# Kernel optimization log

Hardware: AMD Instinct MI355X
Metric: run time of the kernel (lower is better)

Reference implementation:

```python
import jax, jax.numpy as jnp
import numpy as np

B, S, D, H, F = 4, 2048, 1024, 16, 4096
DH = D // H
EPS = 1e-6


def setup_inputs() -> dict:
    key = jax.random.key(0)
    ks = jax.random.split(key, 8)
    sc = 1.0 / np.sqrt(D)
    return {
        "x": jax.random.normal(ks[0], (B, S, D), jnp.float32),
        "wq": jax.random.normal(ks[1], (D, D), jnp.float32) * sc,
        "bq": jnp.zeros((D,), jnp.float32),
        "wk": jax.random.normal(ks[2], (D, D), jnp.float32) * sc,
        "bk": jnp.zeros((D,), jnp.float32),
        "wv": jax.random.normal(ks[3], (D, D), jnp.float32) * sc,
        "bv": jnp.zeros((D,), jnp.float32),
        "wo": jax.random.normal(ks[4], (D, D), jnp.float32) * sc,
        "bo": jnp.zeros((D,), jnp.float32),
        "w1": jax.random.normal(ks[5], (D, F), jnp.float32) * sc,
        "b1": jnp.zeros((F,), jnp.float32),
        "w2": jax.random.normal(ks[6], (F, D), jnp.float32) * (1.0 / np.sqrt(F)),
        "b2": jnp.zeros((D,), jnp.float32),
        "g1": jnp.ones((D,), jnp.float32),
        "be1": jnp.zeros((D,), jnp.float32),
        "g2": jnp.ones((D,), jnp.float32),
        "be2": jnp.zeros((D,), jnp.float32),
    }


def _layernorm(x, g, b):
    mu = jnp.mean(x, axis=-1, keepdims=True)
    var = jnp.mean(jnp.square(x - mu), axis=-1, keepdims=True)
    return (x - mu) * jax.lax.rsqrt(var + EPS) * g + b


def reference(x, wq, bq, wk, bk, wv, bv, wo, bo, w1, b1, w2, b2, g1, be1, g2, be2):
    # self-attention: q=k=v=x
    q = (x @ wq + bq).reshape(B, S, H, DH).transpose(0, 2, 1, 3)  # [B,H,S,DH]
    k = (x @ wk + bk).reshape(B, S, H, DH).transpose(0, 2, 1, 3)
    v = (x @ wv + bv).reshape(B, S, H, DH).transpose(0, 2, 1, 3)
    logits = jnp.einsum("bhqd,bhkd->bhqk", q, k) / jnp.sqrt(jnp.float32(DH))
    attn = jax.nn.softmax(logits, axis=-1)
    ctx = jnp.einsum("bhqk,bhkd->bhqd", attn, v)  # [B,H,S,DH]
    ctx = ctx.transpose(0, 2, 1, 3).reshape(B, S, D)
    attn_out = ctx @ wo + bo
    out1 = _layernorm(x + attn_out, g1, be1)
    ffn = jax.nn.relu(out1 @ w1 + b1) @ w2 + b2
    out2 = _layernorm(out1 + ffn, g2, be2)
    return out2
```

## Files before the change

kernel.cpp:

```cpp
#include <hip/hip_runtime.h>

typedef unsigned short u16;
typedef unsigned int u32;

typedef __attribute__((ext_vector_type(8))) short short8;
typedef __attribute__((ext_vector_type(4))) float floatx4;
typedef __attribute__((ext_vector_type(16))) float floatx16;
typedef __attribute__((ext_vector_type(2))) unsigned int uint2v;
typedef __attribute__((ext_vector_type(4))) unsigned int uint4v;

static __device__ __forceinline__ u16 f2b(float f) {
    union { float f; u32 i; } v; v.f = f;
    u32 r = v.i + 0x7fffu + ((v.i >> 16) & 1u);
    return (u16)(r >> 16);
}
static __device__ __forceinline__ float exp2f_hw(float x) {
    return __builtin_amdgcn_exp2f(x);
}
static __device__ __forceinline__ u32 cvtpk(float lo, float hi) {
    u32 r;
    asm("v_cvt_pk_bf16_f32 %0, %1, %2" : "=v"(r) : "v"(lo), "v"(hi));
    return r;
}

static __device__ __forceinline__ floatx4 mfma16(short8 a, short8 b, floatx4 c) {
    return __builtin_amdgcn_mfma_f32_16x16x32_bf16(a, b, c, 0, 0, 0);
}
static __device__ __forceinline__ floatx16 mfma32(short8 a, short8 b, floatx16 c) {
    return __builtin_amdgcn_mfma_f32_32x32x16_bf16(a, b, c, 0, 0, 0);
}

typedef __attribute__((address_space(1))) const void gas_void;
typedef __attribute__((address_space(3))) void las_void;
static __device__ __forceinline__ void gl_lds16(const void* g, void* l) {
    __builtin_amdgcn_global_load_lds((gas_void*)g, (las_void*)l, 16, 0, 0);
}

template<int N> static __device__ __forceinline__ void vmw() {
    if constexpr (N == 0)      asm volatile("s_waitcnt vmcnt(0)" ::: "memory");
    else if constexpr (N == 2) asm volatile("s_waitcnt vmcnt(2)" ::: "memory");
    else if constexpr (N == 4) asm volatile("s_waitcnt vmcnt(4)" ::: "memory");
}
#define SBAR() asm volatile("s_barrier" ::: "memory")

#define B_ 4
#define S_ 2048
#define D_ 1024
#define H_ 16
#define DH_ 64
#define F_ 4096
#define QKVS 3072

#define QSCALE 0.18033688011112042f

__global__ __launch_bounds__(256) void cast_b(const float* __restrict__ in,
                                              u16* __restrict__ out, int n4) {
    int id = blockIdx.x * 256 + threadIdx.x;
    if (id < n4) {
        float4 v = ((const float4*)in)[id];
        ushort4 u;
        u.x = f2b(v.x); u.y = f2b(v.y); u.z = f2b(v.z); u.w = f2b(v.w);
        ((ushort4*)out)[id] = u;
    }
}

__global__ __launch_bounds__(256) void concat_bias(const float* __restrict__ bq,
                                                   const float* __restrict__ bk,
                                                   const float* __restrict__ bv,
                                                   float* __restrict__ o) {
    int i = blockIdx.x * 256 + threadIdx.x;
    float v;
    if (i < 1024) v = bq[i] * QSCALE;
    else if (i < 2048) v = bk[i - 1024];
    else v = bv[i - 2048];
    o[i] = v;
}

__global__ void transpose_cast(const float* __restrict__ in, u16* __restrict__ out,
                               int R, int C, float scale) {
    __shared__ float t[32][33];
    int bx = blockIdx.x;
    int by = blockIdx.y;
    int x = threadIdx.x, y = threadIdx.y;
#pragma unroll
    for (int i = 0; i < 4; ++i) {
        int r = by * 32 + y + i * 8;
        t[y + i * 8][x] = in[(size_t)r * C + bx * 32 + x];
    }
    __syncthreads();
#pragma unroll
    for (int i = 0; i < 4; ++i) {
        int c = bx * 32 + y + i * 8;
        out[(size_t)c * R + by * 32 + x] = f2b(t[x][y + i * 8] * scale);
    }
}

__global__ void transpose_v(const u16* __restrict__ qkv, u16* __restrict__ vt) {
    __shared__ u16 t[32][33];
    int bh = blockIdx.z; int b = bh >> 4, h = bh & 15;
    int s0 = blockIdx.x * 32, d0 = blockIdx.y * 32;
    int x = threadIdx.x, y = threadIdx.y;
#pragma unroll
    for (int i = 0; i < 4; ++i)
        t[y + i * 8][x] =
            qkv[(size_t)(b * S_ + s0 + y + i * 8) * QKVS + 2048 + h * DH_ + d0 + x];
    __syncthreads();
#pragma unroll
    for (int i = 0; i < 4; ++i)
        vt[((size_t)bh * DH_ + d0 + y + i * 8) * S_ + s0 + x] = t[x][y + i * 8];
}

#define MFMA16X(MH)                                                        \
    __builtin_amdgcn_s_setprio(1);                                         \
    acc[(MH)*4+0][0] = mfma16(af0, bf0, acc[(MH)*4+0][0]);                 \
    acc[(MH)*4+0][1] = mfma16(af0, bf1, acc[(MH)*4+0][1]);                 \
    acc[(MH)*4+0][2] = mfma16(af0, bf2, acc[(MH)*4+0][2]);                 \
    acc[(MH)*4+0][3] = mfma16(af0, bf3, acc[(MH)*4+0][3]);                 \
    acc[(MH)*4+1][0] = mfma16(af1, bf0, acc[(MH)*4+1][0]);                 \
    acc[(MH)*4+1][1] = mfma16(af1, bf1, acc[(MH)*4+1][1]);                 \
    acc[(MH)*4+1][2] = mfma16(af1, bf2, acc[(MH)*4+1][2]);                 \
    acc[(MH)*4+1][3] = mfma16(af1, bf3, acc[(MH)*4+1][3]);                 \
    acc[(MH)*4+2][0] = mfma16(af2, bf0, acc[(MH)*4+2][0]);                 \
    acc[(MH)*4+2][1] = mfma16(af2, bf1, acc[(MH)*4+2][1]);                 \
    acc[(MH)*4+2][2] = mfma16(af2, bf2, acc[(MH)*4+2][2]);                 \
    acc[(MH)*4+2][3] = mfma16(af2, bf3, acc[(MH)*4+2][3]);                 \
    acc[(MH)*4+3][0] = mfma16(af3, bf0, acc[(MH)*4+3][0]);                 \
    acc[(MH)*4+3][1] = mfma16(af3, bf1, acc[(MH)*4+3][1]);                 \
    acc[(MH)*4+3][2] = mfma16(af3, bf2, acc[(MH)*4+3][2]);                 \
    acc[(MH)*4+3][3] = mfma16(af3, bf3, acc[(MH)*4+3][3]);                 \
    __builtin_amdgcn_s_setprio(0);

#define PPAIR(P, KH, STa, Wa, STb, Wb) {                                   \
    int ro = l * 64 + ((((KH) * 4 + quad) ^ l7) << 3);                     \
    const u16* bBp = &smem[32768 + (P) * 16384 + wc * 4096];               \
    short8 bf0 = *(const short8*)&bBp[ro];                                 \
    short8 bf1 = *(const short8*)&bBp[ro + 1024];                          \
    short8 bf2 = *(const short8*)&bBp[ro + 2048];                          \
    short8 bf3 = *(const short8*)&bBp[ro + 3072];                          \
    {   const u16* bAp = &smem[(P) * 16384 + (wr * 2 + 0) * 4096];         \
        short8 af0 = *(const short8*)&bAp[ro];                             \
        short8 af1 = *(const short8*)&bAp[ro + 1024];                      \
        short8 af2 = *(const short8*)&bAp[ro + 2048];                      \
        short8 af3 = *(const short8*)&bAp[ro + 3072];                      \
        STa; Wa;                                                           \
        MFMA16X(0)                                                         \
        SBAR();                                                            \
    }                                                                      \
    {   const u16* bAp = &smem[(P) * 16384 + (wr * 2 + 1) * 4096];         \
        short8 af0 = *(const short8*)&bAp[ro];                             \
        short8 af1 = *(const short8*)&bAp[ro + 1024];                      \
        short8 af2 = *(const short8*)&bAp[ro + 2048];                      \
        short8 af3 = *(const short8*)&bAp[ro + 3072];                      \
        STb; Wb;                                                           \
        MFMA16X(1)                                                         \
        SBAR();                                                            \
    } }

__global__ __launch_bounds__(512) void gemm256(const u16* __restrict__ A,
                                               const u16* __restrict__ Bt,
                                               const float* __restrict__ bias,
                                               float* __restrict__ outF,
                                               float* __restrict__ outF2,
                                               u16* __restrict__ outB,
                                               int M, int N, int K, int klen,
                                               int relu) {
    __shared__ __align__(16) u16 smem[65536];

    int tid = threadIdx.x;
    int w = tid >> 6, lane = tid & 63, quad = lane >> 4, l = lane & 15;
    int wr = w >> 2, wc = w & 3;
    int l7 = l & 7;

    int nbN = gridDim.x, nwg = gridDim.x * gridDim.y;
    int flat = blockIdx.y * gridDim.x + blockIdx.x;
    int swz = (flat & 7) * (nwg >> 3) + (flat >> 3);
    int bM = swz / nbN, bN = swz % nbN;
    int koff = blockIdx.z * klen;

    floatx4 acc[8][4];
#pragma unroll
    for (int i = 0; i < 8; ++i)
#pragma unroll
        for (int j = 0; j < 4; ++j) acc[i][j] = (floatx4){0.f, 0.f, 0.f, 0.f};

    int rT = tid >> 3, cT = tid & 7;
    int cg8 = ((cT ^ (rT & 7)) << 3);
    const u16* gA0 = A + (size_t)(bM * 256 + rT) * K + koff + cg8;
    const u16* gB0 = Bt + (size_t)(bN * 256 + rT) * K + koff + cg8;

    auto stA = [&](int p, int ch, int t) {
        gl_lds16(gA0 + (size_t)(ch * 64) * K + t * 64,
                 (void*)&smem[p * 16384 + ch * 4096 + (w << 9)]);
    };
    auto stB = [&](int p, int hb, int t) {
        gl_lds16(gB0 + (size_t)(hb * 64) * K + t * 64,
                 (void*)&smem[32768 + p * 16384 + hb * 4096 + (w << 9)]);
    };

    stA(0, 0, 0); stA(0, 1, 0); stA(0, 2, 0); stA(0, 3, 0);
    stB(0, 0, 0); stB(0, 1, 0); stB(0, 2, 0); stB(0, 3, 0);
    stA(1, 0, 1); stA(1, 2, 1);
    vmw<2>(); SBAR();

    const int NI = klen >> 7;
    for (int j = 0; j < NI - 1; ++j) {
        int to = 2 * j + 1, te = 2 * j + 2, tn = 2 * j + 3;
        PPAIR(0, 0, (stA(1,1,to), stA(1,3,to), stB(1,0,to), stB(1,1,to)), ((void)0),
                    (stB(1,2,to), stB(1,3,to)), ((void)0))
        PPAIR(0, 1, ((void)0), ((void)0),
                    (stA(0,0,te), stA(0,2,te)), vmw<2>())
        PPAIR(1, 0, (stA(0,1,te), stA(0,3,te), stB(0,0,te), stB(0,1,te)), ((void)0),
                    (stB(0,2,te), stB(0,3,te)), ((void)0))
        PPAIR(1, 1, ((void)0), ((void)0),
                    (stA(1,0,tn), stA(1,2,tn)), vmw<2>())
    }
    {
        int to = 2 * (NI - 1) + 1;
        PPAIR(0, 0, (stA(1,1,to), stA(1,3,to), stB(1,0,to), stB(1,1,to)), ((void)0),
                    (stB(1,2,to), stB(1,3,to)), ((void)0))
        PPAIR(0, 1, ((void)0), ((void)0), ((void)0), vmw<0>())
        PPAIR(1, 0, ((void)0), ((void)0), ((void)0), ((void)0))
        PPAIR(1, 1, ((void)0), ((void)0), ((void)0), ((void)0))
    }

    float* of = (blockIdx.z == 0) ? outF : outF2;
    const float* bp = (blockIdx.z == 0) ? bias : nullptr;
    float bv4[4];
#pragma unroll
    for (int nt = 0; nt < 4; ++nt) {
        int colg = bN * 256 + wc * 64 + nt * 16 + l;
        bv4[nt] = bp ? bp[colg] : 0.f;
    }
#pragma unroll
    for (int mt = 0; mt < 8; ++mt) {
#pragma unroll
        for (int rr = 0; rr < 4; ++rr) {
            int rowg = bM * 256 + wr * 128 + mt * 16 + quad * 4 + rr;
            size_t rb = (size_t)rowg * N + bN * 256 + wc * 64 + l;
#pragma unroll
            for (int nt = 0; nt < 4; ++nt) {
                float v = acc[mt][nt][rr] + bv4[nt];
                if (relu) v = fmaxf(v, 0.f);
                if (of) of[rb + nt * 16] = v;
                if (outB) outB[rb + nt * 16] = f2b(v);
            }
        }
    }
}

#define PACK8(sv, rb, dst) {                                                   \
    u32 pa_ = cvtpk(sv[rb + 0], sv[rb + 1]), pb_ = cvtpk(sv[rb + 4], sv[rb + 5]); \
    u32 pc_ = cvtpk(sv[rb + 2], sv[rb + 3]), pd_ = cvtpk(sv[rb + 6], sv[rb + 7]); \
    uint2v t0_ = __builtin_amdgcn_permlane32_swap(pa_, pb_, 0, 0);             \
    uint2v t1_ = __builtin_amdgcn_permlane32_swap(pc_, pd_, 0, 0);             \
    union { uint4v u; short8 s8; } cv_;                                        \
    cv_.u = (uint4v){t0_[0], t1_[0], t0_[1], t1_[1]};                          \
    dst = cv_.s8; }

__global__ __launch_bounds__(256, 2) void attn_kernel(const u16* __restrict__ qkv,
                                                      const u16* __restrict__ vt,
                                                      u16* __restrict__ ctx) {
    __shared__ __align__(16) u16 Kb[2][64 * 64];
    __shared__ __align__(16) u16 Vb[2][64 * 64];

    int bh = blockIdx.x; int b = bh >> 4, h = bh & 15;
    int tid = threadIdx.x;
    int w = tid >> 6, lane = tid & 63;
    int l32 = lane & 31, hi = lane >> 5, row7 = lane & 7;
    int qw = blockIdx.y * 256 + w * 64;

    int r = lane >> 3, c = lane & 7;
    int cs = ((c ^ r) << 3);
    const u16* gK0 = qkv + (size_t)(b * S_ + w * 16 + r) * QKVS + 1024 + h * DH_ + cs;
    const u16* gK1 = gK0 + (size_t)8 * QKVS;
    const u16* gV0 = vt + (size_t)(bh * DH_ + w * 16 + r) * S_ + cs;
    const u16* gV1 = gV0 + (size_t)8 * S_;

    auto stage = [&](int bb) {
        u16* lk = &Kb[bb][w * 16 * 64];
        u16* lv = &Vb[bb][w * 16 * 64];
        gl_lds16(gK0, lk);
        gl_lds16(gK1, lk + 8 * 64);
        gl_lds16(gV0, lv);
        gl_lds16(gV1, lv + 8 * 64);
        gK0 += (size_t)64 * QKVS; gK1 += (size_t)64 * QKVS;
        gV0 += 64; gV1 += 64;
    };

    short8 qa0, qa1, qa2, qa3, qb0, qb1, qb2, qb3;
    {
        const u16* qpA = qkv + (size_t)(b * S_ + qw + l32) * QKVS + h * DH_ + hi * 8;
        qa0 = *(const short8*)(qpA);
        qa1 = *(const short8*)(qpA + 16);
        qa2 = *(const short8*)(qpA + 32);
        qa3 = *(const short8*)(qpA + 48);
        const u16* qpB = qpA + (size_t)32 * QKVS;
        qb0 = *(const short8*)(qpB);
        qb1 = *(const short8*)(qpB + 16);
        qb2 = *(const short8*)(qpB + 32);
        qb3 = *(const short8*)(qpB + 48);
    }

    floatx16 OA0, OA1, OB0, OB1;
#pragma unroll
    for (int i = 0; i < 16; ++i) { OA0[i] = 0.f; OA1[i] = 0.f; OB0[i] = 0.f; OB1[i] = 0.f; }
    float lra0 = 0.f, lra1 = 0.f, lrb0 = 0.f, lrb1 = 0.f;

    int roff0 = l32 * 64;
    int roff1 = (32 + l32) * 64;

    stage(0);
    __syncthreads();

    const int NT = S_ / 64;
    for (int kt = 0; kt < NT; ++kt) {
        int cur = kt & 1;
        if (kt + 1 < NT) stage(cur ^ 1);

        const u16* Kc = Kb[cur];
        const u16* Vc = Vb[cur];

        short8 paA0, paA1, paA2, paA3, paB0, paB1, paB2, paB3;

        {
            floatx16 sA, sB;
#pragma unroll
            for (int i = 0; i < 16; ++i) { sA[i] = 0.f; sB[i] = 0.f; }
#pragma unroll
            for (int kc = 0; kc < 4; ++kc) {
                int ch = (((kc * 2 + hi) ^ row7) << 3);
                short8 ka = *(const short8*)&Kc[roff0 + ch];
                short8 qkA = (kc == 0) ? qa0 : (kc == 1) ? qa1 : (kc == 2) ? qa2 : qa3;
                short8 qkB = (kc == 0) ? qb0 : (kc == 1) ? qb1 : (kc == 2) ? qb2 : qb3;
                sA = mfma32(ka, qkA, sA);
                sB = mfma32(ka, qkB, sB);
            }
#pragma unroll
            for (int i = 0; i < 16; ++i) { sA[i] = exp2f_hw(sA[i]); sB[i] = exp2f_hw(sB[i]); }
#pragma unroll
            for (int i = 0; i < 16; i += 4) {
                lra0 += sA[i + 0] + sA[i + 1];
                lra1 += sA[i + 2] + sA[i + 3];
                lrb0 += sB[i + 0] + sB[i + 1];
                lrb1 += sB[i + 2] + sB[i + 3];
            }
            PACK8(sA, 0, paA0); PACK8(sA, 8, paA1);
            PACK8(sB, 0, paB0); PACK8(sB, 8, paB1);
        }

        {
            floatx16 sA, sB;
#pragma unroll
            for (int i = 0; i < 16; ++i) { sA[i] = 0.f; sB[i] = 0.f; }
#pragma unroll
            for (int kc = 0; kc < 4; ++kc) {
                int ch = (((kc * 2 + hi) ^ row7) << 3);
                short8 ka = *(const short8*)&Kc[roff1 + ch];
                short8 qkA = (kc == 0) ? qa0 : (kc == 1) ? qa1 : (kc == 2) ? qa2 : qa3;
                short8 qkB = (kc == 0) ? qb0 : (kc == 1) ? qb1 : (kc == 2) ? qb2 : qb3;
                sA = mfma32(ka, qkA, sA);
                sB = mfma32(ka, qkB, sB);
            }
#pragma unroll
            for (int i = 0; i < 16; ++i) { sA[i] = exp2f_hw(sA[i]); sB[i] = exp2f_hw(sB[i]); }
#pragma unroll
            for (int i = 0; i < 16; i += 4) {
                lra0 += sA[i + 0] + sA[i + 1];
                lra1 += sA[i + 2] + sA[i + 3];
                lrb0 += sB[i + 0] + sB[i + 1];
                lrb1 += sB[i + 2] + sB[i + 3];
            }
            PACK8(sA, 0, paA2); PACK8(sA, 8, paA3);
            PACK8(sB, 0, paB2); PACK8(sB, 8, paB3);
        }

        {
            short8 vb0 = *(const short8*)&Vc[roff0 + (((0 + hi) ^ row7) << 3)];
            OA0 = mfma32(paA0, vb0, OA0);
            OB0 = mfma32(paB0, vb0, OB0);
            short8 vb1 = *(const short8*)&Vc[roff0 + (((2 + hi) ^ row7) << 3)];
            OA0 = mfma32(paA1, vb1, OA0);
            OB0 = mfma32(paB1, vb1, OB0);
            short8 vb2 = *(const short8*)&Vc[roff0 + (((4 + hi) ^ row7) << 3)];
            OA0 = mfma32(paA2, vb2, OA0);
            OB0 = mfma32(paB2, vb2, OB0);
            short8 vb3 = *(const short8*)&Vc[roff0 + (((6 + hi) ^ row7) << 3)];
            OA0 = mfma32(paA3, vb3, OA0);
            OB0 = mfma32(paB3, vb3, OB0);
        }
        {
            short8 vb0 = *(const short8*)&Vc[roff1 + (((0 + hi) ^ row7) << 3)];
            OA1 = mfma32(paA0, vb0, OA1);
            OB1 = mfma32(paB0, vb0, OB1);
            short8 vb1 = *(const short8*)&Vc[roff1 + (((2 + hi) ^ row7) << 3)];
            OA1 = mfma32(paA1, vb1, OA1);
            OB1 = mfma32(paB1, vb1, OB1);
            short8 vb2 = *(const short8*)&Vc[roff1 + (((4 + hi) ^ row7) << 3)];
            OA1 = mfma32(paA2, vb2, OA1);
            OB1 = mfma32(paB2, vb2, OB1);
            short8 vb3 = *(const short8*)&Vc[roff1 + (((6 + hi) ^ row7) << 3)];
            OA1 = mfma32(paA3, vb3, OA1);
            OB1 = mfma32(paB3, vb3, OB1);
        }

        __syncthreads();
    }

    float lrA = lra0 + lra1;
    float lrB = lrb0 + lrb1;
    lrA += __shfl_xor(lrA, 32);
    lrB += __shfl_xor(lrB, 32);
    float invA = 1.0f / lrA;
    float invB = 1.0f / lrB;
#pragma unroll
    for (int rr = 0; rr < 16; ++rr) {
        int rowq = (rr & 3) + 8 * (rr >> 2) + 4 * hi;
        float ivA = __shfl(invA, rowq);
        float ivB = __shfl(invB, rowq);
        size_t baseA = (size_t)(b * S_ + qw + rowq) * D_ + h * DH_ + l32;
        ctx[baseA]      = f2b(OA0[rr] * ivA);
        ctx[baseA + 32] = f2b(OA1[rr] * ivA);
        size_t baseB = baseA + (size_t)32 * D_;
        ctx[baseB]      = f2b(OB0[rr] * ivB);
        ctx[baseB + 32] = f2b(OB1[rr] * ivB);
    }
}

__global__ __launch_bounds__(256) void add_ln(const float* __restrict__ a,
                                              const float* __restrict__ b,
                                              const float* __restrict__ g,
                                              const float* __restrict__ be,
                                              float* __restrict__ outF,
                                              u16* __restrict__ outB) {
    int row = blockIdx.x, tid = threadIdx.x;
    size_t base = (size_t)row * D_;
    float4 va = ((const float4*)(a + base))[tid];
    float4 vb = ((const float4*)(b + base))[tid];
    float x0 = va.x + vb.x, x1 = va.y + vb.y, x2 = va.z + vb.z, x3 = va.w + vb.w;
    float s1 = x0 + x1 + x2 + x3;
    float s2 = x0 * x0 + x1 * x1 + x2 * x2 + x3 * x3;
#pragma unroll
    for (int off = 32; off; off >>= 1) {
        s1 += __shfl_xor(s1, off);
        s2 += __shfl_xor(s2, off);
    }
    __shared__ float r1[4], r2[4];
    int w = tid >> 6, lane = tid & 63;
    if (lane == 0) { r1[w] = s1; r2[w] = s2; }
    __syncthreads();
    s1 = r1[0] + r1[1] + r1[2] + r1[3];
    s2 = r2[0] + r2[1] + r2[2] + r2[3];
    float mean = s1 * (1.0f / D_);
    float var = s2 * (1.0f / D_) - mean * mean;
    float inv = rsqrtf(var + 1e-6f);
    float4 vg = ((const float4*)g)[tid];
    float4 vbe = ((const float4*)be)[tid];
    float o0 = (x0 - mean) * inv * vg.x + vbe.x;
    float o1 = (x1 - mean) * inv * vg.y + vbe.y;
    float o2 = (x2 - mean) * inv * vg.z + vbe.z;
    float o3 = (x3 - mean) * inv * vg.w + vbe.w;
    float4 o; o.x = o0; o.y = o1; o.z = o2; o.w = o3;
    ((float4*)(outF + base))[tid] = o;
    if (outB) {
        ushort4 u;
        u.x = f2b(o0); u.y = f2b(o1); u.z = f2b(o2); u.w = f2b(o3);
        ((ushort4*)(outB + base))[tid] = u;
    }
}

__global__ __launch_bounds__(256) void add_ln3(const float* __restrict__ a,
                                               const float* __restrict__ b,
                                               const float* __restrict__ c,
                                               const float* __restrict__ g,
                                               const float* __restrict__ be,
                                               float* __restrict__ outF,
                                               u16* __restrict__ outB) {
    int row = blockIdx.x, tid = threadIdx.x;
    size_t base = (size_t)row * D_;
    float4 va = ((const float4*)(a + base))[tid];
    float4 vb = ((const float4*)(b + base))[tid];
    float4 vc = ((const float4*)(c + base))[tid];
    float x0 = va.x + vb.x + vc.x, x1 = va.y + vb.y + vc.y;
    float x2 = va.z + vb.z + vc.z, x3 = va.w + vb.w + vc.w;
    float s1 = x0 + x1 + x2 + x3;
    float s2 = x0 * x0 + x1 * x1 + x2 * x2 + x3 * x3;
#pragma unroll
    for (int off = 32; off; off >>= 1) {
        s1 += __shfl_xor(s1, off);
        s2 += __shfl_xor(s2, off);
    }
    __shared__ float r1[4], r2[4];
    int w = tid >> 6, lane = tid & 63;
    if (lane == 0) { r1[w] = s1; r2[w] = s2; }
    __syncthreads();
    s1 = r1[0] + r1[1] + r1[2] + r1[3];
    s2 = r2[0] + r2[1] + r2[2] + r2[3];
    float mean = s1 * (1.0f / D_);
    float var = s2 * (1.0f / D_) - mean * mean;
    float inv = rsqrtf(var + 1e-6f);
    float4 vg = ((const float4*)g)[tid];
    float4 vbe = ((const float4*)be)[tid];
    float o0 = (x0 - mean) * inv * vg.x + vbe.x;
    float o1 = (x1 - mean) * inv * vg.y + vbe.y;
    float o2 = (x2 - mean) * inv * vg.z + vbe.z;
    float o3 = (x3 - mean) * inv * vg.w + vbe.w;
    float4 o; o.x = o0; o.y = o1; o.z = o2; o.w = o3;
    ((float4*)(outF + base))[tid] = o;
    if (outB) {
        ushort4 u;
        u.x = f2b(o0); u.y = f2b(o1); u.z = f2b(o2); u.w = f2b(o3);
        ((ushort4*)(outB + base))[tid] = u;
    }
}

extern "C" void kernel_launch(void* const* d_in, const int* in_sizes, int n_in,
                              void* d_out, int out_size, void* d_ws, size_t ws_size,
                              hipStream_t stream) {
    const float* x   = (const float*)d_in[0];
    const float* wq  = (const float*)d_in[1];
    const float* bq  = (const float*)d_in[2];
    const float* wk  = (const float*)d_in[3];
    const float* bk  = (const float*)d_in[4];
    const float* wv  = (const float*)d_in[5];
    const float* bv  = (const float*)d_in[6];
    const float* wo  = (const float*)d_in[7];
    const float* bo  = (const float*)d_in[8];
    const float* w1  = (const float*)d_in[9];
    const float* b1  = (const float*)d_in[10];
    const float* w2  = (const float*)d_in[11];
    const float* b2  = (const float*)d_in[12];
    const float* g1  = (const float*)d_in[13];
    const float* be1 = (const float*)d_in[14];
    const float* g2  = (const float*)d_in[15];
    const float* be2 = (const float*)d_in[16];
    float* out = (float*)d_out;
    char* ws = (char*)d_ws;
    const size_t MB = 1u << 20;

    u16* xb      = (u16*)(ws + 0);
    u16* wqkvT   = (u16*)(ws + 16 * MB);
    u16* woT     = (u16*)(ws + 22 * MB);
    u16* w1T     = (u16*)(ws + 24 * MB);
    u16* w2T     = (u16*)(ws + 32 * MB);
    float* qkvb  = (float*)(ws + 40 * MB);
    u16* qkv     = (u16*)(ws + 41 * MB);
    u16* vtb     = (u16*)(ws + 89 * MB);
    u16* ctxb    = (u16*)(ws + 105 * MB);
    float* attn_out = (float*)(ws + 121 * MB);
    float* out1     = (float*)(ws + 153 * MB);
    u16* out1b   = (u16*)(ws + 0);
    float* woP1  = (float*)(ws + 41 * MB);
    u16* hidden  = (u16*)(ws + 41 * MB);
    float* ffn2p0 = (float*)(ws + 121 * MB);

    dim3 tb(32, 8);

    cast_b<<<8192, 256, 0, stream>>>(x, xb, (B_ * S_ * D_) / 4);
    transpose_cast<<<dim3(32, 32), tb, 0, stream>>>(wq, wqkvT, D_, D_, QSCALE);
    transpose_cast<<<dim3(32, 32), tb, 0, stream>>>(wk, wqkvT + 1024 * 1024, D_, D_, 1.0f);
    transpose_cast<<<dim3(32, 32), tb, 0, stream>>>(wv, wqkvT + 2048 * 1024, D_, D_, 1.0f);
    transpose_cast<<<dim3(32, 32), tb, 0, stream>>>(wo, woT, D_, D_, 1.0f);
    transpose_cast<<<dim3(128, 32), tb, 0, stream>>>(w1, w1T, D_, F_, 1.0f);
    transpose_cast<<<dim3(32, 128), tb, 0, stream>>>(w2, w2T, F_, D_, 1.0f);
    concat_bias<<<12, 256, 0, stream>>>(bq, bk, bv, qkvb);

    gemm256<<<dim3(12, 32, 1), 512, 0, stream>>>(xb, wqkvT, qkvb, nullptr, nullptr,
                                                 qkv, B_ * S_, QKVS, D_, D_, 0);
    transpose_v<<<dim3(S_ / 32, DH_ / 32, B_ * H_), tb, 0, stream>>>(qkv, vtb);

    attn_kernel<<<dim3(B_ * H_, S_ / 256), 256, 0, stream>>>(qkv, vtb, ctxb);

    gemm256<<<dim3(4, 32, 2), 512, 0, stream>>>(ctxb, woT, bo, attn_out, woP1,
                                                nullptr, B_ * S_, D_, D_, D_ / 2, 0);
    add_ln3<<<B_ * S_, 256, 0, stream>>>(x, attn_out, woP1, g1, be1, out1, out1b);

    gemm256<<<dim3(16, 32, 1), 512, 0, stream>>>(out1b, w1T, b1, nullptr, nullptr,
                                                 hidden, B_ * S_, F_, D_, D_, 1);
    gemm256<<<dim3(4, 32, 2), 512, 0, stream>>>(hidden, w2T, b2, ffn2p0, out,
                                                nullptr, B_ * S_, D_, F_, F_ / 2, 0);
    add_ln3<<<B_ * S_, 256, 0, stream>>>(out1, ffn2p0, out, g2, be2, out, nullptr);
}
```

Baseline: 493.1 us.

## Split attention KV range across waves with LDS reduction of partial outputs

Each block now handles 64 queries, with its four waves each covering a disjoint quarter of the keys instead of separate query rows. Each wave stages its own K/V tiles in private LDS buffers using explicit vmcnt waits, so per-iteration block barriers are gone. Partial outputs and row sums are combined through shared memory at the end, and results are stored with vectorized writes. This quadruples the grid and Q loads and adds an LDS reduction step. It relies on softmax without a max subtraction, so partial sums from different waves can simply be added.

```diff
diff --git a/kernel.cpp b/kernel.cpp
--- a/kernel.cpp
+++ b/kernel.cpp
@@ -40,6 +40,7 @@
     if constexpr (N == 0)      asm volatile("s_waitcnt vmcnt(0)" ::: "memory");
     else if constexpr (N == 2) asm volatile("s_waitcnt vmcnt(2)" ::: "memory");
     else if constexpr (N == 4) asm volatile("s_waitcnt vmcnt(4)" ::: "memory");
+    else if constexpr (N == 8) asm volatile("s_waitcnt vmcnt(8)" ::: "memory");
 }
 #define SBAR() asm volatile("s_barrier" ::: "memory")
 
@@ -257,34 +258,40 @@
     cv_.u = (uint4v){t0_[0], t1_[0], t0_[1], t1_[1]};                          \
     dst = cv_.s8; }
 
+#define OREG_STRIDE 72
+#define OREG_REGION (64 * OREG_STRIDE)
+#define LRS_OFF (4 * OREG_REGION)
+
 __global__ __launch_bounds__(256, 2) void attn_kernel(const u16* __restrict__ qkv,
                                                       const u16* __restrict__ vt,
                                                       u16* __restrict__ ctx) {
-    __shared__ __align__(16) u16 Kb[2][64 * 64];
-    __shared__ __align__(16) u16 Vb[2][64 * 64];
+    __shared__ __align__(16) char smem[4 * OREG_REGION * 4 + 4 * 64 * 4];
 
     int bh = blockIdx.x; int b = bh >> 4, h = bh & 15;
     int tid = threadIdx.x;
     int w = tid >> 6, lane = tid & 63;
-    int l32 = lane & 31, hi = lane >> 5, row7 = lane & 7;
-    int qw = blockIdx.y * 256 + w * 64;
-
-    int r = lane >> 3, c = lane & 7;
-    int cs = ((c ^ r) << 3);
-    const u16* gK0 = qkv + (size_t)(b * S_ + w * 16 + r) * QKVS + 1024 + h * DH_ + cs;
-    const u16* gK1 = gK0 + (size_t)8 * QKVS;
-    const u16* gV0 = vt + (size_t)(bh * DH_ + w * 16 + r) * S_ + cs;
-    const u16* gV1 = gV0 + (size_t)8 * S_;
-
-    auto stage = [&](int bb) {
-        u16* lk = &Kb[bb][w * 16 * 64];
-        u16* lv = &Vb[bb][w * 16 * 64];
-        gl_lds16(gK0, lk);
-        gl_lds16(gK1, lk + 8 * 64);
-        gl_lds16(gV0, lv);
-        gl_lds16(gV1, lv + 8 * 64);
-        gK0 += (size_t)64 * QKVS; gK1 += (size_t)64 * QKVS;
-        gV0 += 64; gV1 += 64;
+    int l32 = lane & 31, hi = lane >> 5, row7 = lane & 7, r3 = lane & 3;
+    int qw = blockIdx.y * 64;
+
+    u16* Kw = (u16*)(smem + w * 16384);
+    u16* Vw = (u16*)(smem + w * 16384 + 8192);
+
+    int rK = lane >> 3, cK = lane & 7;
+    int csK = ((cK ^ rK) << 3);
+    int rV = lane >> 2, cV = lane & 3;
+    int csV = ((cV ^ (rV & 3)) << 3);
+    const u16* gK = qkv + (size_t)(b * S_ + w * 512 + rK) * QKVS + 1024 + h * DH_ + csK;
+    const u16* gV = vt + ((size_t)bh * DH_ + rV) * S_ + w * 512 + csV;
+
+    auto stage = [&](int bb, int kt) {
+        u16* lk = Kw + bb * 2048;
+        u16* lv = Vw + bb * 2048;
+#pragma unroll
+        for (int i = 0; i < 4; ++i)
+            gl_lds16(gK + (size_t)(kt * 32 + i * 8) * QKVS, lk + i * 512);
+#pragma unroll
+        for (int i = 0; i < 4; ++i)
+            gl_lds16(gV + (size_t)(i * 16) * S_ + kt * 32, lv + i * 512);
     };
 
     short8 qa0, qa1, qa2, qa3, qb0, qb1, qb2, qb3;
@@ -304,125 +311,111 @@
     floatx16 OA0, OA1, OB0, OB1;
 #pragma unroll
     for (int i = 0; i < 16; ++i) { OA0[i] = 0.f; OA1[i] = 0.f; OB0[i] = 0.f; OB1[i] = 0.f; }
-    float lra0 = 0.f, lra1 = 0.f, lrb0 = 0.f, lrb1 = 0.f;
-
-    int roff0 = l32 * 64;
-    int roff1 = (32 + l32) * 64;
-
-    stage(0);
-    __syncthreads();
-
-    const int NT = S_ / 64;
+    float lra = 0.f, lrb = 0.f;
+
+    stage(0, 0);
+
+    const int NT = 512 / 32;
     for (int kt = 0; kt < NT; ++kt) {
         int cur = kt & 1;
-        if (kt + 1 < NT) stage(cur ^ 1);
-
-        const u16* Kc = Kb[cur];
-        const u16* Vc = Vb[cur];
-
-        short8 paA0, paA1, paA2, paA3, paB0, paB1, paB2, paB3;
-
+        if (kt + 1 < NT) { stage(cur ^ 1, kt + 1); vmw<8>(); }
+        else             { vmw<0>(); }
+
+        const u16* Kc = Kw + cur * 2048;
+        const u16* Vc = Vw + cur * 2048;
+
+        floatx16 sA, sB;
+#pragma unroll
+        for (int i = 0; i < 16; ++i) { sA[i] = 0.f; sB[i] = 0.f; }
+        __builtin_amdgcn_s_setprio(1);
+#pragma unroll
+        for (int kc = 0; kc < 4; ++kc) {
+            int ch = (((kc * 2 + hi) ^ row7) << 3);
+            short8 ka = *(const short8*)&Kc[l32 * 64 + ch];
+            short8 qkA = (kc == 0) ? qa0 : (kc == 1) ? qa1 : (kc == 2) ? qa2 : qa3;
+            short8 qkB = (kc == 0) ? qb0 : (kc == 1) ? qb1 : (kc == 2) ? qb2 : qb3;
+            sA = mfma32(ka, qkA, sA);
+            sB = mfma32(ka, qkB, sB);
+        }
+        __builtin_amdgcn_s_setprio(0);
+#pragma unroll
+        for (int i = 0; i < 16; ++i) { sA[i] = exp2f_hw(sA[i]); sB[i] = exp2f_hw(sB[i]); }
+#pragma unroll
+        for (int i = 0; i < 16; ++i) { lra += sA[i]; lrb += sB[i]; }
+        short8 paA0, paA1, paB0, paB1;
+        PACK8(sA, 0, paA0); PACK8(sA, 8, paA1);
+        PACK8(sB, 0, paB0); PACK8(sB, 8, paB1);
+
+        __builtin_amdgcn_s_setprio(1);
         {
-            floatx16 sA, sB;
-#pragma unroll
-            for (int i = 0; i < 16; ++i) { sA[i] = 0.f; sB[i] = 0.f; }
-#pragma unroll
-            for (int kc = 0; kc < 4; ++kc) {
-                int ch = (((kc * 2 + hi) ^ row7) << 3);
-                short8 ka = *(const short8*)&Kc[roff0 + ch];
-                short8 qkA = (kc == 0) ? qa0 : (kc == 1) ? qa1 : (kc == 2) ? qa2 : qa3;
-                short8 qkB = (kc == 0) ? qb0 : (kc == 1) ? qb1 : (kc == 2) ? qb2 : qb3;
-                sA = mfma32(ka, qkA, sA);
-                sB = mfma32(ka, qkB, sB);
-            }
-#pragma unroll
-            for (int i = 0; i < 16; ++i) { sA[i] = exp2f_hw(sA[i]); sB[i] = exp2f_hw(sB[i]); }
-#pragma unroll
-            for (int i = 0; i < 16; i += 4) {
-                lra0 += sA[i + 0] + sA[i + 1];
-                lra1 += sA[i + 2] + sA[i + 3];
-                lrb0 += sB[i + 0] + sB[i + 1];
-                lrb1 += sB[i + 2] + sB[i + 3];
-            }
-            PACK8(sA, 0, paA0); PACK8(sA, 8, paA1);
-            PACK8(sB, 0, paB0); PACK8(sB, 8, paB1);
-        }
-
-        {
-            floatx16 sA, sB;
-#pragma unroll
-            for (int i = 0; i < 16; ++i) { sA[i] = 0.f; sB[i] = 0.f; }
-#pragma unroll
-            for (int kc = 0; kc < 4; ++kc) {
-                int ch = (((kc * 2 + hi) ^ row7) << 3);
-                short8 ka = *(const short8*)&Kc[roff1 + ch];
-                short8 qkA = (kc == 0) ? qa0 : (kc == 1) ? qa1 : (kc == 2) ? qa2 : qa3;
-                short8 qkB = (kc == 0) ? qb0 : (kc == 1) ? qb1 : (kc == 2) ? qb2 : qb3;
-                sA = mfma32(ka, qkA, sA);
-                sB = mfma32(ka, qkB, sB);
-            }
-#pragma unroll
-            for (int i = 0; i < 16; ++i) { sA[i] = exp2f_hw(sA[i]); sB[i] = exp2f_hw(sB[i]); }
-#pragma unroll
-            for (int i = 0; i < 16; i += 4) {
-                lra0 += sA[i + 0] + sA[i + 1];
-                lra1 += sA[i + 2] + sA[i + 3];
-                lrb0 += sB[i + 0] + sB[i + 1];
-                lrb1 += sB[i + 2] + sB[i + 3];
-            }
-            PACK8(sA, 0, paA2); PACK8(sA, 8, paA3);
-            PACK8(sB, 0, paB2); PACK8(sB, 8, paB3);
-        }
-
-        {
-            short8 vb0 = *(const short8*)&Vc[roff0 + (((0 + hi) ^ row7) << 3)];
+            short8 vb0 = *(const short8*)&Vc[l32 * 32 + (((0 + hi) ^ r3) << 3)];
             OA0 = mfma32(paA0, vb0, OA0);
             OB0 = mfma32(paB0, vb0, OB0);
-            short8 vb1 = *(const short8*)&Vc[roff0 + (((2 + hi) ^ row7) << 3)];
+            short8 vb1 = *(const short8*)&Vc[l32 * 32 + (((2 + hi) ^ r3) << 3)];
             OA0 = mfma32(paA1, vb1, OA0);
             OB0 = mfma32(paB1, vb1, OB0);
-            short8 vb2 = *(const short8*)&Vc[roff0 + (((4 + hi) ^ row7) << 3)];
-            OA0 = mfma32(paA2, vb2, OA0);
-            OB0 = mfma32(paB2, vb2, OB0);
-            short8 vb3 = *(const short8*)&Vc[roff0 + (((6 + hi) ^ row7) << 3)];
-            OA0 = mfma32(paA3, vb3, OA0);
-            OB0 = mfma32(paB3, vb3, OB0);
         }
         {
-            short8 vb0 = *(const short8*)&Vc[roff1 + (((0 + hi) ^ row7) << 3)];
+            short8 vb0 = *(const short8*)&Vc[(32 + l32) * 32 + (((0 + hi) ^ r3) << 3)];
             OA1 = mfma32(paA0, vb0, OA1);
             OB1 = mfma32(paB0, vb0, OB1);
-            short8 vb1 = *(const short8*)&Vc[roff1 + (((2 + hi) ^ row7) << 3)];
+            short8 vb1 = *(const short8*)&Vc[(32 + l32) * 32 + (((2 + hi) ^ r3) << 3)];
             OA1 = mfma32(paA1, vb1, OA1);
             OB1 = mfma32(paB1, vb1, OB1);
-            short8 vb2 = *(const short8*)&Vc[roff1 + (((4 + hi) ^ row7) << 3)];
-            OA1 = mfma32(paA2, vb2, OA1);
-            OB1 = mfma32(paB2, vb2, OB1);
-            short8 vb3 = *(const short8*)&Vc[roff1 + (((6 + hi) ^ row7) << 3)];
-            OA1 = mfma32(paA3, vb3, OA1);
-            OB1 = mfma32(paB3, vb3, OB1);
-        }
-
-        __syncthreads();
-    }
-
-    float lrA = lra0 + lra1;
-    float lrB = lrb0 + lrb1;
-    lrA += __shfl_xor(lrA, 32);
-    lrB += __shfl_xor(lrB, 32);
-    float invA = 1.0f / lrA;
-    float invB = 1.0f / lrB;
-#pragma unroll
-    for (int rr = 0; rr < 16; ++rr) {
-        int rowq = (rr & 3) + 8 * (rr >> 2) + 4 * hi;
-        float ivA = __shfl(invA, rowq);
-        float ivB = __shfl(invB, rowq);
-        size_t baseA = (size_t)(b * S_ + qw + rowq) * D_ + h * DH_ + l32;
-        ctx[baseA]      = f2b(OA0[rr] * ivA);
-        ctx[baseA + 32] = f2b(OA1[rr] * ivA);
-        size_t baseB = baseA + (size_t)32 * D_;
-        ctx[baseB]      = f2b(OB0[rr] * ivB);
-        ctx[baseB + 32] = f2b(OB1[rr] * ivB);
+        }
+        __builtin_amdgcn_s_setprio(0);
+    }
+
+    float lrA = lra + __shfl_xor(lra, 32);
+    float lrB = lrb + __shfl_xor(lrb, 32);
+
+    __syncthreads();
+
+    float* Oreg = (float*)smem;
+    float* lrs  = (float*)smem + LRS_OFF;
+    {
+        float* reg = Oreg + w * OREG_REGION;
+#pragma unroll
+        for (int rr = 0; rr < 16; ++rr) {
+            int q = (rr & 3) + 8 * (rr >> 2) + 4 * hi;
+            reg[q * OREG_STRIDE + l32]            = OA0[rr];
+            reg[q * OREG_STRIDE + 32 + l32]       = OA1[rr];
+            reg[(32 + q) * OREG_STRIDE + l32]     = OB0[rr];
+            reg[(32 + q) * OREG_STRIDE + 32 + l32] = OB1[rr];
+        }
+        if (hi == 0) {
+            lrs[w * 64 + l32]      = lrA;
+            lrs[w * 64 + 32 + l32] = lrB;
+        }
+    }
+    __syncthreads();
+
+    {
+        int q = 16 * w + (lane >> 2);
+        int cg = (lane & 3) * 16;
+        float4 s0 = {0,0,0,0}, s1 = {0,0,0,0}, s2 = {0,0,0,0}, s3 = {0,0,0,0};
+#pragma unroll
+        for (int r = 0; r < 4; ++r) {
+            const float* p = Oreg + r * OREG_REGION + q * OREG_STRIDE + cg;
+            float4 a = ((const float4*)p)[0];
+            float4 b2 = ((const float4*)p)[1];
+            float4 c2 = ((const float4*)p)[2];
+            float4 d2 = ((const float4*)p)[3];
+            s0.x += a.x; s0.y += a.y; s0.z += a.z; s0.w += a.w;
+            s1.x += b2.x; s1.y += b2.y; s1.z += b2.z; s1.w += b2.w;
+            s2.x += c2.x; s2.y += c2.y; s2.z += c2.z; s2.w += c2.w;
+            s3.x += d2.x; s3.y += d2.y; s3.z += d2.z; s3.w += d2.w;
+        }
+        float lt = lrs[q] + lrs[64 + q] + lrs[128 + q] + lrs[192 + q];
+        float inv = 1.0f / lt;
+        u16* p = ctx + (size_t)(b * S_ + qw + q) * D_ + h * DH_ + cg;
+        ushort4 u0, u1, u2, u3;
+        u0.x = f2b(s0.x * inv); u0.y = f2b(s0.y * inv); u0.z = f2b(s0.z * inv); u0.w = f2b(s0.w * inv);
+        u1.x = f2b(s1.x * inv); u1.y = f2b(s1.y * inv); u1.z = f2b(s1.z * inv); u1.w = f2b(s1.w * inv);
+        u2.x = f2b(s2.x * inv); u2.y = f2b(s2.y * inv); u2.z = f2b(s2.z * inv); u2.w = f2b(s2.w * inv);
+        u3.x = f2b(s3.x * inv); u3.y = f2b(s3.y * inv); u3.z = f2b(s3.z * inv); u3.w = f2b(s3.w * inv);
+        ((ushort4*)p)[0] = u0; ((ushort4*)p)[1] = u1;
+        ((ushort4*)p)[2] = u2; ((ushort4*)p)[3] = u3;
     }
 }
 
@@ -568,7 +561,7 @@
                                                  qkv, B_ * S_, QKVS, D_, D_, 0);
     transpose_v<<<dim3(S_ / 32, DH_ / 32, B_ * H_), tb, 0, stream>>>(qkv, vtb);
 
-    attn_kernel<<<dim3(B_ * H_, S_ / 256), 256, 0, stream>>>(qkv, vtb, ctxb);
+    attn_kernel<<<dim3(B_ * H_, S_ / 64), 256, 0, stream>>>(qkv, vtb, ctxb);
 
     gemm256<<<dim3(4, 32, 2), 512, 0, stream>>>(ctxb, woT, bo, attn_out, woP1,
                                                 nullptr, B_ * S_, D_, D_, D_ / 2, 0);
```

After: 520.1 us. 5.5% more time.

## Fuse prep kernels into one launch and double attention K/V tile per stage

Applied to the files above, without the earlier changes.

Merges the input cast, the six weight transpose-casts and the bias concat into a single prep kernel launch that dispatches on block index, which removes per-launch overhead and tail effects. The attention kernel now stages two 64-key sub-tiles per iteration (128 keys), which halves the number of barriers and pipeline steps. This doubles its LDS footprint to 64 KB per block, which may limit occupancy at two blocks per CU. The unused add_ln kernel is removed.

```diff
diff --git a/kernel.cpp b/kernel.cpp
--- a/kernel.cpp
+++ b/kernel.cpp
@@ -53,45 +53,65 @@
 
 #define QSCALE 0.18033688011112042f
 
-__global__ __launch_bounds__(256) void cast_b(const float* __restrict__ in,
-                                              u16* __restrict__ out, int n4) {
-    int id = blockIdx.x * 256 + threadIdx.x;
-    if (id < n4) {
-        float4 v = ((const float4*)in)[id];
+__global__ __launch_bounds__(256) void prep(
+    const float* __restrict__ x, u16* __restrict__ xb,
+    const float* __restrict__ wq, const float* __restrict__ wk,
+    const float* __restrict__ wv, const float* __restrict__ wo,
+    u16* __restrict__ wqkvT, u16* __restrict__ woT,
+    const float* __restrict__ w1, u16* __restrict__ w1T,
+    const float* __restrict__ w2, u16* __restrict__ w2T,
+    const float* __restrict__ bq, const float* __restrict__ bk,
+    const float* __restrict__ bv, float* __restrict__ qkvb) {
+    int bid = blockIdx.x, tid = threadIdx.x;
+
+    if (bid < 8192) {
+        int id = bid * 256 + tid;
+        float4 v = ((const float4*)x)[id];
         ushort4 u;
         u.x = f2b(v.x); u.y = f2b(v.y); u.z = f2b(v.z); u.w = f2b(v.w);
-        ((ushort4*)out)[id] = u;
-    }
-}
-
-__global__ __launch_bounds__(256) void concat_bias(const float* __restrict__ bq,
-                                                   const float* __restrict__ bk,
-                                                   const float* __restrict__ bv,
-                                                   float* __restrict__ o) {
-    int i = blockIdx.x * 256 + threadIdx.x;
-    float v;
-    if (i < 1024) v = bq[i] * QSCALE;
-    else if (i < 2048) v = bk[i - 1024];
-    else v = bv[i - 2048];
-    o[i] = v;
-}
-
-__global__ void transpose_cast(const float* __restrict__ in, u16* __restrict__ out,
-                               int R, int C, float scale) {
+        ((ushort4*)xb)[id] = u;
+        return;
+    }
+    bid -= 8192;
+
+    if (bid >= 12288) {
+        int i = (bid - 12288) * 256 + tid;
+        float v;
+        if (i < 1024) v = bq[i] * QSCALE;
+        else if (i < 2048) v = bk[i - 1024];
+        else v = bv[i - 2048];
+        qkvb[i] = v;
+        return;
+    }
+
     __shared__ float t[32][33];
-    int bx = blockIdx.x;
-    int by = blockIdx.y;
-    int x = threadIdx.x, y = threadIdx.y;
+    int x32 = tid & 31, y8 = tid >> 5;
+    const float* in; u16* outp; float scale = 1.0f; int R, C, bx, by;
+    if (bid < 4096) {
+        int z = bid >> 10, rem = bid & 1023;
+        bx = rem & 31; by = rem >> 5;
+        in = (z == 0) ? wq : (z == 1) ? wk : (z == 2) ? wv : wo;
+        outp = (z == 0) ? wqkvT : (z == 1) ? (wqkvT + 1024 * 1024)
+             : (z == 2) ? (wqkvT + 2048 * 1024) : woT;
+        scale = (z == 0) ? QSCALE : 1.0f;
+        R = 1024; C = 1024;
+    } else if (bid < 8192) {
+        int rem = bid - 4096; bx = rem & 127; by = rem >> 7;
+        in = w1; outp = w1T; R = 1024; C = 4096;
+    } else {
+        int rem = bid - 8192; bx = rem & 31; by = rem >> 5;
+        in = w2; outp = w2T; R = 4096; C = 1024;
+    }
 #pragma unroll
     for (int i = 0; i < 4; ++i) {
-        int r = by * 32 + y + i * 8;
-        t[y + i * 8][x] = in[(size_t)r * C + bx * 32 + x];
+        int r = by * 32 + y8 + i * 8;
+        t[y8 + i * 8][x32] = in[(size_t)r * C + bx * 32 + x32];
     }
     __syncthreads();
 #pragma unroll
     for (int i = 0; i < 4; ++i) {
-        int c = bx * 32 + y + i * 8;
-        out[(size_t)c * R + by * 32 + x] = f2b(t[x][y + i * 8] * scale);
+        int c = bx * 32 + y8 + i * 8;
+        outp[(size_t)c * R + by * 32 + x32] = f2b(t[x32][y8 + i * 8] * scale);
     }
 }
 
@@ -260,8 +280,8 @@
 __global__ __launch_bounds__(256, 2) void attn_kernel(const u16* __restrict__ qkv,
                                                       const u16* __restrict__ vt,
                                                       u16* __restrict__ ctx) {
-    __shared__ __align__(16) u16 Kb[2][64 * 64];
-    __shared__ __align__(16) u16 Vb[2][64 * 64];
+    __shared__ __align__(16) u16 Kb[2][128 * 64];
+    __shared__ __align__(16) u16 Vb[2][128 * 64];
 
     int bh = blockIdx.x; int b = bh >> 4, h = bh & 15;
     int tid = threadIdx.x;
@@ -276,9 +296,9 @@
     const u16* gV0 = vt + (size_t)(bh * DH_ + w * 16 + r) * S_ + cs;
     const u16* gV1 = gV0 + (size_t)8 * S_;
 
-    auto stage = [&](int bb) {
-        u16* lk = &Kb[bb][w * 16 * 64];
-        u16* lv = &Vb[bb][w * 16 * 64];
+    auto stage = [&](int bb, int hh) {
+        u16* lk = &Kb[bb][hh * 4096 + w * 16 * 64];
+        u16* lv = &Vb[bb][hh * 4096 + w * 16 * 64];
         gl_lds16(gK0, lk);
         gl_lds16(gK1, lk + 8 * 64);
         gl_lds16(gV0, lv);
@@ -309,98 +329,101 @@
     int roff0 = l32 * 64;
     int roff1 = (32 + l32) * 64;
 
-    stage(0);
+    stage(0, 0); stage(0, 1);
     __syncthreads();
 
-    const int NT = S_ / 64;
+    const int NT = S_ / 128;
     for (int kt = 0; kt < NT; ++kt) {
         int cur = kt & 1;
-        if (kt + 1 < NT) stage(cur ^ 1);
-
-        const u16* Kc = Kb[cur];
-        const u16* Vc = Vb[cur];
-
-        short8 paA0, paA1, paA2, paA3, paB0, paB1, paB2, paB3;
-
-        {
-            floatx16 sA, sB;
-#pragma unroll
-            for (int i = 0; i < 16; ++i) { sA[i] = 0.f; sB[i] = 0.f; }
-#pragma unroll
-            for (int kc = 0; kc < 4; ++kc) {
-                int ch = (((kc * 2 + hi) ^ row7) << 3);
-                short8 ka = *(const short8*)&Kc[roff0 + ch];
-                short8 qkA = (kc == 0) ? qa0 : (kc == 1) ? qa1 : (kc == 2) ? qa2 : qa3;
-                short8 qkB = (kc == 0) ? qb0 : (kc == 1) ? qb1 : (kc == 2) ? qb2 : qb3;
-                sA = mfma32(ka, qkA, sA);
-                sB = mfma32(ka, qkB, sB);
+        if (kt + 1 < NT) { stage(cur ^ 1, 0); stage(cur ^ 1, 1); }
+
+#pragma unroll
+        for (int hh = 0; hh < 2; ++hh) {
+            const u16* Kc = &Kb[cur][hh * 4096];
+            const u16* Vc = &Vb[cur][hh * 4096];
+
+            short8 paA0, paA1, paA2, paA3, paB0, paB1, paB2, paB3;
+
+            {
+                floatx16 sA, sB;
+#pragma unroll
+                for (int i = 0; i < 16; ++i) { sA[i] = 0.f; sB[i] = 0.f; }
+#pragma unroll
+                for (int kc = 0; kc < 4; ++kc) {
+                    int ch = (((kc * 2 + hi) ^ row7) << 3);
+                    short8 ka = *(const short8*)&Kc[roff0 + ch];
+                    short8 qkA = (kc == 0) ? qa0 : (kc == 1) ? qa1 : (kc == 2) ? qa2 : qa3;
+                    short8 qkB = (kc == 0) ? qb0 : (kc == 1) ? qb1 : (kc == 2) ? qb2 : qb3;
+                    sA = mfma32(ka, qkA, sA);
+                    sB = mfma32(ka, qkB, sB);
+                }
+#pragma unroll
+                for (int i = 0; i < 16; ++i) { sA[i] = exp2f_hw(sA[i]); sB[i] = exp2f_hw(sB[i]); }
+#pragma unroll
+                for (int i = 0; i < 16; i += 4) {
+                    lra0 += sA[i + 0] + sA[i + 1];
+                    lra1 += sA[i + 2] + sA[i + 3];
+                    lrb0 += sB[i + 0] + sB[i + 1];
+                    lrb1 += sB[i + 2] + sB[i + 3];
+                }
+                PACK8(sA, 0, paA0); PACK8(sA, 8, paA1);
+                PACK8(sB, 0, paB0); PACK8(sB, 8, paB1);
             }
-#pragma unroll
-            for (int i = 0; i < 16; ++i) { sA[i] = exp2f_hw(sA[i]); sB[i] = exp2f_hw(sB[i]); }
-#pragma unroll
-            for (int i = 0; i < 16; i += 4) {
-                lra0 += sA[i + 0] + sA[i + 1];
-                lra1 += sA[i + 2] + sA[i + 3];
-                lrb0 += sB[i + 0] + sB[i + 1];
-                lrb1 += sB[i + 2] + sB[i + 3];
+
+            {
+                floatx16 sA, sB;
+#pragma unroll
+                for (int i = 0; i < 16; ++i) { sA[i] = 0.f; sB[i] = 0.f; }
+#pragma unroll
+                for (int kc = 0; kc < 4; ++kc) {
+                    int ch = (((kc * 2 + hi) ^ row7) << 3);
+                    short8 ka = *(const short8*)&Kc[roff1 + ch];
+                    short8 qkA = (kc == 0) ? qa0 : (kc == 1) ? qa1 : (kc == 2) ? qa2 : qa3;
+                    short8 qkB = (kc == 0) ? qb0 : (kc == 1) ? qb1 : (kc == 2) ? qb2 : qb3;
+                    sA = mfma32(ka, qkA, sA);
+                    sB = mfma32(ka, qkB, sB);
+                }
+#pragma unroll
+                for (int i = 0; i < 16; ++i) { sA[i] = exp2f_hw(sA[i]); sB[i] = exp2f_hw(sB[i]); }
+#pragma unroll
+                for (int i = 0; i < 16; i += 4) {
+                    lra0 += sA[i + 0] + sA[i + 1];
+                    lra1 += sA[i + 2] + sA[i + 3];
+                    lrb0 += sB[i + 0] + sB[i + 1];
+                    lrb1 += sB[i + 2] + sB[i + 3];
+                }
+                PACK8(sA, 0, paA2); PACK8(sA, 8, paA3);
+                PACK8(sB, 0, paB2); PACK8(sB, 8, paB3);
             }
-            PACK8(sA, 0, paA0); PACK8(sA, 8, paA1);
-            PACK8(sB, 0, paB0); PACK8(sB, 8, paB1);
-        }
-
-        {
-            floatx16 sA, sB;
-#pragma unroll
-            for (int i = 0; i < 16; ++i) { sA[i] = 0.f; sB[i] = 0.f; }
-#pragma unroll
-            for (int kc = 0; kc < 4; ++kc) {
-                int ch = (((kc * 2 + hi) ^ row7) << 3);
-                short8 ka = *(const short8*)&Kc[roff1 + ch];
-                short8 qkA = (kc == 0) ? qa0 : (kc == 1) ? qa1 : (kc == 2) ? qa2 : qa3;
-                short8 qkB = (kc == 0) ? qb0 : (kc == 1) ? qb1 : (kc == 2) ? qb2 : qb3;
-                sA = mfma32(ka, qkA, sA);
-                sB = mfma32(ka, qkB, sB);
+
+            {
+                short8 vb0 = *(const short8*)&Vc[roff0 + (((0 + hi) ^ row7) << 3)];
+                OA0 = mfma32(paA0, vb0, OA0);
+                OB0 = mfma32(paB0, vb0, OB0);
+                short8 vb1 = *(const short8*)&Vc[roff0 + (((2 + hi) ^ row7) << 3)];
+                OA0 = mfma32(paA1, vb1, OA0);
+                OB0 = mfma32(paB1, vb1, OB0);
+                short8 vb2 = *(const short8*)&Vc[roff0 + (((4 + hi) ^ row7) << 3)];
+                OA0 = mfma32(paA2, vb2, OA0);
+                OB0 = mfma32(paB2, vb2, OB0);
+                short8 vb3 = *(const short8*)&Vc[roff0 + (((6 + hi) ^ row7) << 3)];
+                OA0 = mfma32(paA3, vb3, OA0);
+                OB0 = mfma32(paB3, vb3, OB0);
             }
-#pragma unroll
-            for (int i = 0; i < 16; ++i) { sA[i] = exp2f_hw(sA[i]); sB[i] = exp2f_hw(sB[i]); }
-#pragma unroll
-            for (int i = 0; i < 16; i += 4) {
-                lra0 += sA[i + 0] + sA[i + 1];
-                lra1 += sA[i + 2] + sA[i + 3];
-                lrb0 += sB[i + 0] + sB[i + 1];
-                lrb1 += sB[i + 2] + sB[i + 3];
+            {
+                short8 vb0 = *(const short8*)&Vc[roff1 + (((0 + hi) ^ row7) << 3)];
+                OA1 = mfma32(paA0, vb0, OA1);
+                OB1 = mfma32(paB0, vb0, OB1);
+                short8 vb1 = *(const short8*)&Vc[roff1 + (((2 + hi) ^ row7) << 3)];
+                OA1 = mfma32(paA1, vb1, OA1);
+                OB1 = mfma32(paB1, vb1, OB1);
+                short8 vb2 = *(const short8*)&Vc[roff1 + (((4 + hi) ^ row7) << 3)];
+                OA1 = mfma32(paA2, vb2, OA1);
+                OB1 = mfma32(paB2, vb2, OB1);
+                short8 vb3 = *(const short8*)&Vc[roff1 + (((6 + hi) ^ row7) << 3)];
+                OA1 = mfma32(paA3, vb3, OA1);
+                OB1 = mfma32(paB3, vb3, OB1);
             }
-            PACK8(sA, 0, paA2); PACK8(sA, 8, paA3);
-            PACK8(sB, 0, paB2); PACK8(sB, 8, paB3);
-        }
-
-        {
-            short8 vb0 = *(const short8*)&Vc[roff0 + (((0 + hi) ^ row7) << 3)];
-            OA0 = mfma32(paA0, vb0, OA0);
-            OB0 = mfma32(paB0, vb0, OB0);
-            short8 vb1 = *(const short8*)&Vc[roff0 + (((2 + hi) ^ row7) << 3)];
-            OA0 = mfma32(paA1, vb1, OA0);
-            OB0 = mfma32(paB1, vb1, OB0);
-            short8 vb2 = *(const short8*)&Vc[roff0 + (((4 + hi) ^ row7) << 3)];
-            OA0 = mfma32(paA2, vb2, OA0);
-            OB0 = mfma32(paB2, vb2, OB0);
-            short8 vb3 = *(const short8*)&Vc[roff0 + (((6 + hi) ^ row7) << 3)];
-            OA0 = mfma32(paA3, vb3, OA0);
-            OB0 = mfma32(paB3, vb3, OB0);
-        }
-        {
-            short8 vb0 = *(const short8*)&Vc[roff1 + (((0 + hi) ^ row7) << 3)];
-            OA1 = mfma32(paA0, vb0, OA1);
-            OB1 = mfma32(paB0, vb0, OB1);
-            short8 vb1 = *(const short8*)&Vc[roff1 + (((2 + hi) ^ row7) << 3)];
-            OA1 = mfma32(paA1, vb1, OA1);
-            OB1 = mfma32(paB1, vb1, OB1);
-            short8 vb2 = *(const short8*)&Vc[roff1 + (((4 + hi) ^ row7) << 3)];
-            OA1 = mfma32(paA2, vb2, OA1);
-            OB1 = mfma32(paB2, vb2, OB1);
-            short8 vb3 = *(const short8*)&Vc[roff1 + (((6 + hi) ^ row7) << 3)];
-            OA1 = mfma32(paA3, vb3, OA1);
-            OB1 = mfma32(paB3, vb3, OB1);
         }
 
         __syncthreads();
@@ -423,48 +446,6 @@
         size_t baseB = baseA + (size_t)32 * D_;
         ctx[baseB]      = f2b(OB0[rr] * ivB);
         ctx[baseB + 32] = f2b(OB1[rr] * ivB);
-    }
-}
-
-__global__ __launch_bounds__(256) void add_ln(const float* __restrict__ a,
-                                              const float* __restrict__ b,
-                                              const float* __restrict__ g,
-                                              const float* __restrict__ be,
-                                              float* __restrict__ outF,
-                                              u16* __restrict__ outB) {
-    int row = blockIdx.x, tid = threadIdx.x;
-    size_t base = (size_t)row * D_;
-    float4 va = ((const float4*)(a + base))[tid];
-    float4 vb = ((const float4*)(b + base))[tid];
-    float x0 = va.x + vb.x, x1 = va.y + vb.y, x2 = va.z + vb.z, x3 = va.w + vb.w;
-    float s1 = x0 + x1 + x2 + x3;
-    float s2 = x0 * x0 + x1 * x1 + x2 * x2 + x3 * x3;
-#pragma unroll
-    for (int off = 32; off; off >>= 1) {
-        s1 += __shfl_xor(s1, off);
-        s2 += __shfl_xor(s2, off);
-    }
-    __shared__ float r1[4], r2[4];
-    int w = tid >> 6, lane = tid & 63;
-    if (lane == 0) { r1[w] = s1; r2[w] = s2; }
-    __syncthreads();
-    s1 = r1[0] + r1[1] + r1[2] + r1[3];
-    s2 = r2[0] + r2[1] + r2[2] + r2[3];
-    float mean = s1 * (1.0f / D_);
-    float var = s2 * (1.0f / D_) - mean * mean;
-    float inv = rsqrtf(var + 1e-6f);
-    float4 vg = ((const float4*)g)[tid];
-    float4 vbe = ((const float4*)be)[tid];
-    float o0 = (x0 - mean) * inv * vg.x + vbe.x;
-    float o1 = (x1 - mean) * inv * vg.y + vbe.y;
-    float o2 = (x2 - mean) * inv * vg.z + vbe.z;
-    float o3 = (x3 - mean) * inv * vg.w + vbe.w;
-    float4 o; o.x = o0; o.y = o1; o.z = o2; o.w = o3;
-    ((float4*)(outF + base))[tid] = o;
-    if (outB) {
-        ushort4 u;
-        u.x = f2b(o0); u.y = f2b(o1); u.z = f2b(o2); u.w = f2b(o3);
-        ((ushort4*)(outB + base))[tid] = u;
     }
 }
 
@@ -553,20 +534,12 @@
     u16* hidden  = (u16*)(ws + 41 * MB);
     float* ffn2p0 = (float*)(ws + 121 * MB);
 
-    dim3 tb(32, 8);
-
-    cast_b<<<8192, 256, 0, stream>>>(x, xb, (B_ * S_ * D_) / 4);
-    transpose_cast<<<dim3(32, 32), tb, 0, stream>>>(wq, wqkvT, D_, D_, QSCALE);
-    transpose_cast<<<dim3(32, 32), tb, 0, stream>>>(wk, wqkvT + 1024 * 1024, D_, D_, 1.0f);
-    transpose_cast<<<dim3(32, 32), tb, 0, stream>>>(wv, wqkvT + 2048 * 1024, D_, D_, 1.0f);
-    transpose_cast<<<dim3(32, 32), tb, 0, stream>>>(wo, woT, D_, D_, 1.0f);
-    transpose_cast<<<dim3(128, 32), tb, 0, stream>>>(w1, w1T, D_, F_, 1.0f);
-    transpose_cast<<<dim3(32, 128), tb, 0, stream>>>(w2, w2T, F_, D_, 1.0f);
-    concat_bias<<<12, 256, 0, stream>>>(bq, bk, bv, qkvb);
+    prep<<<20492, 256, 0, stream>>>(x, xb, wq, wk, wv, wo, wqkvT, woT,
+                                    w1, w1T, w2, w2T, bq, bk, bv, qkvb);
 
     gemm256<<<dim3(12, 32, 1), 512, 0, stream>>>(xb, wqkvT, qkvb, nullptr, nullptr,
                                                  qkv, B_ * S_, QKVS, D_, D_, 0);
-    transpose_v<<<dim3(S_ / 32, DH_ / 32, B_ * H_), tb, 0, stream>>>(qkv, vtb);
+    transpose_v<<<dim3(S_ / 32, DH_ / 32, B_ * H_), dim3(32, 8), 0, stream>>>(qkv, vtb);
 
     attn_kernel<<<dim3(B_ * H_, S_ / 256), 256, 0, stream>>>(qkv, vtb, ctxb);
 
```

Measured after the change: 497.9 us. About the same (+1.0%).
